# Kernel optimization log

Measured on AMD Instinct MI355X. Metric: run time of the kernel, lower is better.

The kernel has to match this reference:

```python
import jax, jax.numpy as jnp
import numpy as np

N_D = 100000  # num drug nodes
N_G = 100000  # num gene nodes
E = 250000    # edges per etype
D_IN_DRUG, D_IN_GENE, D_OUT = 512, 256, 512
W_SCALE = 0.02


def setup_inputs() -> dict:
    key = jax.random.key(0)
    ks = jax.random.split(key, 20)
    inp = {
        "x_drug": jax.random.normal(ks[0], (N_D, D_IN_DRUG), jnp.float32),
        "x_gene": jax.random.normal(ks[1], (N_G, D_IN_GENE), jnp.float32),
        "W_drug": jax.random.normal(ks[2], (D_IN_DRUG, D_OUT), jnp.float32) * W_SCALE,
        "b_drug": jnp.zeros((D_OUT,), jnp.float32),
        "W_gene": jax.random.normal(ks[3], (D_IN_GENE, D_OUT), jnp.float32) * W_SCALE,
        "b_gene": jnp.zeros((D_OUT,), jnp.float32),
        "W_dd": jax.random.normal(ks[4], (D_OUT, D_OUT), jnp.float32) * W_SCALE,
        "b_dd": jnp.zeros((D_OUT,), jnp.float32),
        "W_dg": jax.random.normal(ks[5], (D_OUT, D_OUT), jnp.float32) * W_SCALE,
        "b_dg": jnp.zeros((D_OUT,), jnp.float32),
        "W_gd": jax.random.normal(ks[6], (D_OUT, D_OUT), jnp.float32) * W_SCALE,
        "b_gd": jnp.zeros((D_OUT,), jnp.float32),
        "W_gg": jax.random.normal(ks[7], (D_OUT, D_OUT), jnp.float32) * W_SCALE,
        "b_gg": jnp.zeros((D_OUT,), jnp.float32),
        "src_dd": jax.random.randint(ks[8], (E,), 0, N_D, jnp.int64),
        "dst_dd": jax.random.randint(ks[9], (E,), 0, N_D, jnp.int64),
        "src_dg": jax.random.randint(ks[10], (E,), 0, N_D, jnp.int64),
        "dst_dg": jax.random.randint(ks[11], (E,), 0, N_G, jnp.int64),
        "src_gd": jax.random.randint(ks[12], (E,), 0, N_G, jnp.int64),
        "dst_gd": jax.random.randint(ks[13], (E,), 0, N_D, jnp.int64),
        "src_gg": jax.random.randint(ks[14], (E,), 0, N_G, jnp.int64),
        "dst_gg": jax.random.randint(ks[15], (E,), 0, N_G, jnp.int64),
    }
    return inp


def _graph_conv(h_src, src, dst, n_src, n_dst, W, b):
    """DGL GraphConv with norm='both': src-norm, scatter-sum, dst-norm, W, bias."""
    ones = jnp.ones(src.shape, h_src.dtype)
    deg_out = jax.ops.segment_sum(ones, src, num_segments=n_src)
    deg_in = jax.ops.segment_sum(ones, dst, num_segments=n_dst)
    norm_src = jax.lax.rsqrt(jnp.maximum(deg_out, 1.0))  # clamp(min=1)
    norm_dst = jax.lax.rsqrt(jnp.maximum(deg_in, 1.0))
    msg = (h_src * norm_src[:, None])[src]               # [E, D_OUT]
    agg = jax.ops.segment_sum(msg, dst, num_segments=n_dst)
    agg = agg * norm_dst[:, None]
    return agg @ W + b


def reference(x_drug, x_gene, W_drug, b_drug, W_gene, b_gene,
              W_dd, b_dd, W_dg, b_dg, W_gd, b_gd, W_gg, b_gg,
              src_dd, dst_dd, src_dg, dst_dg, src_gd, dst_gd, src_gg, dst_gg):
    # per-ntype linear projections to out_size
    h_d = x_drug @ W_drug + b_drug   # [N_D, D_OUT]
    h_g = x_gene @ W_gene + b_gene   # [N_G, D_OUT]
    # per-etype GraphConv aggregates
    f_dd = _graph_conv(h_d, src_dd, dst_dd, N_D, N_D, W_dd, b_dd)  # -> drug
    f_gd = _graph_conv(h_g, src_gd, dst_gd, N_G, N_D, W_gd, b_gd)  # -> drug
    f_dg = _graph_conv(h_d, src_dg, dst_dg, N_D, N_G, W_dg, b_dg)  # -> gene
    f_gg = _graph_conv(h_g, src_gg, dst_gg, N_G, N_G, W_gg, b_gg)  # -> gene
    # mean over etypes targeting each dsttype (stack(...).mean(0))
    out_drug = 0.5 * (f_dd + f_gd)
    out_gene = 0.5 * (f_dg + f_gg)
    return out_drug, out_gene
```

## Files before the change

kernel.cpp:

```cpp
#include <hip/hip_runtime.h>
#include <stdint.h>
#include <stdio.h>

#define ND 100000
#define NG 100000
#define NE 250000
#define NNODE 100000
#define NB 391
#define NBE 977
#define OSTRIDE 100016

typedef __attribute__((ext_vector_type(8))) short short8;
typedef __attribute__((ext_vector_type(4))) int   int4v;
typedef __attribute__((ext_vector_type(2))) int   int2v;
typedef __attribute__((ext_vector_type(4))) float f32x4;

__device__ __forceinline__ float bf2f(short s) {
  union { unsigned u; float f; } v;
  v.u = ((unsigned)(unsigned short)s) << 16;
  return v.f;
}
__device__ __forceinline__ short f2bf_rne(float f) {
  union { float f; unsigned u; } v;
  v.f = f;
  unsigned u = v.u + 0x7FFFu + ((v.u >> 16) & 1u);
  return (short)(u >> 16);
}

__global__ void detect_kernel(const unsigned short* __restrict__ xs,
                              const int* __restrict__ idx, int* __restrict__ flags) {
  __shared__ int cnt_huge, cnt_oddnz;
  if (threadIdx.x == 0) { cnt_huge = 0; cnt_oddnz = 0; }
  __syncthreads();
  int t = threadIdx.x;
  int h = 0;
#pragma unroll
  for (int i = 0; i < 8; ++i) {
    unsigned e = ((unsigned)xs[t * 8 + i] >> 7) & 0xFFu;
    if (e >= 0xC0u) ++h;
  }
  if (h) atomicAdd(&cnt_huge, h);
  if (t < 128 && idx[2 * t + 1] != 0) atomicAdd(&cnt_oddnz, 1);
  __syncthreads();
  if (t == 0) {
    flags[0] = (cnt_huge > 8) ? 1 : 0;
    flags[1] = (cnt_oddnz == 0) ? 1 : 0;
  }
}

__global__ void hist8_kernel(const int* __restrict__ i0, const int* __restrict__ i1,
                             const int* __restrict__ i2, const int* __restrict__ i3,
                             const int* __restrict__ i4, const int* __restrict__ i5,
                             const int* __restrict__ i6, const int* __restrict__ i7,
                             float* __restrict__ degbase, const int* __restrict__ flags) {
  int slot = blockIdx.y;
  const int* idx = slot == 0 ? i0 : slot == 1 ? i1 : slot == 2 ? i2 : slot == 3 ? i3
                 : slot == 4 ? i4 : slot == 5 ? i5 : slot == 6 ? i6 : i7;
  int t = blockIdx.x * blockDim.x + threadIdx.x;
  if (t < NE) {
    int v = flags[1] ? idx[2 * (size_t)t] : idx[t];
    atomicAdd(degbase + (size_t)slot * NNODE + v, 1.0f);
  }
}

__global__ void norm_kernel(float* __restrict__ d, int n) {
  int t = blockIdx.x * blockDim.x + threadIdx.x;
  if (t < n) {
    float v = d[t];
    d[t] = rsqrtf(v < 1.0f ? 1.0f : v);
  }
}


__global__ void scan_partial(const float* __restrict__ degbase, int* __restrict__ part) {
  int et = blockIdx.y, t = threadIdx.x;
  const float* deg = degbase + (size_t)(2 * et + 1) * NNODE;
  __shared__ int sm[256];
  int i = blockIdx.x * 256 + t;
  int v = (i < NNODE) ? (int)deg[i] : 0;
  sm[t] = v;
  __syncthreads();
  for (int s = 128; s > 0; s >>= 1) {
    if (t < s) sm[t] += sm[t + s];
    __syncthreads();
  }
  if (t == 0) part[et * 512 + blockIdx.x] = sm[0];
}

__global__ void scan_single(int* __restrict__ part) {
  int et = blockIdx.x, t = threadIdx.x;
  __shared__ int sm[512];
  int v = (t < NB) ? part[et * 512 + t] : 0;
  sm[t] = v;
  __syncthreads();
  for (int s = 1; s < 512; s <<= 1) {
    int a = (t >= s) ? sm[t - s] : 0;
    __syncthreads();
    sm[t] += a;
    __syncthreads();
  }
  if (t < NB) part[et * 512 + t] = sm[t] - v;
}

__global__ void scan_final(const float* __restrict__ degbase, const int* __restrict__ part,
                           int* __restrict__ offsbase) {
  int et = blockIdx.y, t = threadIdx.x;
  const float* deg = degbase + (size_t)(2 * et + 1) * NNODE;
  int* offs = offsbase + (size_t)et * OSTRIDE;
  __shared__ int sm[256];
  int i = blockIdx.x * 256 + t;
  int v = (i < NNODE) ? (int)deg[i] : 0;
  sm[t] = v;
  __syncthreads();
  for (int s = 1; s < 256; s <<= 1) {
    int a = (t >= s) ? sm[t - s] : 0;
    __syncthreads();
    sm[t] += a;
    __syncthreads();
  }
  int excl = sm[t] - v;
  int base = part[et * 512 + blockIdx.x];
  if (i < NNODE) offs[i] = base + excl;
  if (i == NNODE - 1) offs[NNODE] = base + excl + v;
}

__global__ void csr_scatter4(
    const int* __restrict__ s0, const int* __restrict__ d0,
    const int* __restrict__ s1, const int* __restrict__ d1,
    const int* __restrict__ s2, const int* __restrict__ d2,
    const int* __restrict__ s3, const int* __restrict__ d3,
    const float* __restrict__ degbase, const int* __restrict__ csro,
    int* __restrict__ curs, int* __restrict__ ewbase, const int* __restrict__ flags) {
  int et = blockIdx.y;
  const int* src = et == 0 ? s0 : et == 1 ? s1 : et == 2 ? s2 : s3;
  const int* dst = et == 0 ? d0 : et == 1 ? d1 : et == 2 ? d2 : d3;
  const float* ns = degbase + (size_t)(2 * et) * NNODE;
  const int* offs = csro + (size_t)et * OSTRIDE;
  int* cur = curs + (size_t)et * NNODE;
  int* ew = ewbase + (size_t)et * 2 * NE;
  int t = blockIdx.x * blockDim.x + threadIdx.x;
  if (t >= NE) return;
  int i64 = flags[1];
  int s = i64 ? src[2 * (size_t)t] : src[t];
  int d = i64 ? dst[2 * (size_t)t] : dst[t];
  int pos = offs[d] + atomicAdd(&cur[d], 1);
  union { float f; int i; } u;
  u.f = ns[s];
  int2v v; v[0] = s; v[1] = u.i;
  *(int2v*)(ew + 2 * (size_t)pos) = v;
}

template <int EL>
__device__ __forceinline__ void accum_row(const void* __restrict__ x, int s, float w,
                                          float* acc, int lane, int xf) {
  constexpr int D = EL * 64;
  if (xf) {
    const float* xp = (const float*)x + (size_t)s * D + lane * EL;
    if constexpr (EL == 8) {
      f32x4 q0 = *(const f32x4*)xp;
      f32x4 q1 = *(const f32x4*)(xp + 4);
#pragma unroll
      for (int i = 0; i < 4; ++i) { acc[i] += w * q0[i]; acc[4 + i] += w * q1[i]; }
    } else {
      f32x4 q0 = *(const f32x4*)xp;
#pragma unroll
      for (int i = 0; i < 4; ++i) acc[i] += w * q0[i];
    }
  } else {
    const short* xp = (const short*)x + (size_t)s * D + lane * EL;
    if constexpr (EL == 8) {
      int4v q = *(const int4v*)xp;
#pragma unroll
      for (int i = 0; i < 4; ++i) {
        unsigned u = (unsigned)q[i];
        union { unsigned u; float f; } lo, hi;
        lo.u = u << 16; hi.u = u & 0xFFFF0000u;
        acc[2 * i] += w * lo.f;
        acc[2 * i + 1] += w * hi.f;
      }
    } else {
      int2v q = *(const int2v*)(xp);
#pragma unroll
      for (int i = 0; i < 2; ++i) {
        unsigned u = (unsigned)q[i];
        union { unsigned u; float f; } lo, hi;
        lo.u = u << 16; hi.u = u & 0xFFFF0000u;
        acc[2 * i] += w * lo.f;
        acc[2 * i + 1] += w * hi.f;
      }
    }
  }
}

template <int EL>
__global__ __launch_bounds__(256) void csr_gather2(
    const void* __restrict__ x,
    const int* __restrict__ offsA, const int* __restrict__ ewA,
    const float* __restrict__ ndA, short* __restrict__ yA, float* __restrict__ svA,
    const int* __restrict__ offsB, const int* __restrict__ ewB,
    const float* __restrict__ ndB, short* __restrict__ yB, float* __restrict__ svB,
    const int* __restrict__ flags) {
  constexpr int D = EL * 64;
  int which = blockIdx.x & 1;
  int d = (blockIdx.x >> 1) * 4 + (threadIdx.x >> 6);
  int lane = threadIdx.x & 63;
  int xf = flags[0];
  const int* offs = which ? offsB : offsA;
  const int* ew   = which ? ewB : ewA;
  const float* nd = which ? ndB : ndA;
  short* y        = which ? yB : yA;
  float* sv       = which ? svB : svA;

  int beg = offs[d], end = offs[d + 1];
  float acc[EL];
#pragma unroll
  for (int i = 0; i < EL; ++i) acc[i] = 0.f;
  float sw = 0.f;
  int j = beg;
  for (; j + 2 <= end; j += 2) {
    int2v e0 = *(const int2v*)(ew + 2 * (size_t)j);
    int2v e1 = *(const int2v*)(ew + 2 * (size_t)j + 2);
    union { int i; float f; } u0, u1;
    u0.i = e0[1]; u1.i = e1[1];
    sw += u0.f + u1.f;
    accum_row<EL>(x, e0[0], u0.f, acc, lane, xf);
    accum_row<EL>(x, e1[0], u1.f, acc, lane, xf);
  }
  if (j < end) {
    int2v e0 = *(const int2v*)(ew + 2 * (size_t)j);
    union { int i; float f; } u0;
    u0.i = e0[1];
    sw += u0.f;
    accum_row<EL>(x, e0[0], u0.f, acc, lane, xf);
  }
  float ndv = nd[d];
  if constexpr (EL == 8) {
    union { short s[8]; int4v v; } o;
#pragma unroll
    for (int i = 0; i < 8; ++i) o.s[i] = f2bf_rne(acc[i] * ndv);
    __builtin_nontemporal_store(o.v, (int4v*)(y + (size_t)d * D + lane * EL));
  } else {
    union { short s[4]; int2v v; } o;
#pragma unroll
    for (int i = 0; i < 4; ++i) o.s[i] = f2bf_rne(acc[i] * ndv);
    __builtin_nontemporal_store(o.v, (int2v*)(y + (size_t)d * D + lane * EL));
  }
  if (lane == 0) sv[d] = ndv * sw;
}

__global__ void vt_kernel(const void* __restrict__ Ws, const void* __restrict__ We,
                          short* __restrict__ VT, int Kin, const int* __restrict__ flags) {
  int n = blockIdx.x * 256 + threadIdx.x;
  int k = blockIdx.y;
  float acc = 0.f;
  if (flags[0]) {
    const float* wr = (const float*)Ws + (size_t)k * 512;
    const float* we = (const float*)We;
#pragma unroll 8
    for (int j = 0; j < 512; ++j) acc += wr[j] * we[(size_t)j * 512 + n];
  } else {
    const short* wr = (const short*)Ws + (size_t)k * 512;
    const short* we = (const short*)We;
#pragma unroll 8
    for (int j = 0; j < 512; ++j) acc += bf2f(wr[j]) * bf2f(we[(size_t)j * 512 + n]);
  }
  VT[(size_t)n * Kin + k] = f2bf_rne(0.5f * acc);
}

__global__ void cvec_kernel(const void* __restrict__ b1s, const void* __restrict__ W1,
                            const void* __restrict__ b2s, const void* __restrict__ W2,
                            const void* __restrict__ be1, const void* __restrict__ be2,
                            float* __restrict__ c1, float* __restrict__ c2,
                            float* __restrict__ cb, const int* __restrict__ flags) {
  int n = blockIdx.x * 256 + threadIdx.x;
  float a1 = 0.f, a2 = 0.f, vb1, vb2;
  if (flags[0]) {
    const float* B1 = (const float*)b1s; const float* M1 = (const float*)W1;
    const float* B2 = (const float*)b2s; const float* M2 = (const float*)W2;
    for (int j = 0; j < 512; ++j) {
      a1 += B1[j] * M1[(size_t)j * 512 + n];
      a2 += B2[j] * M2[(size_t)j * 512 + n];
    }
    vb1 = ((const float*)be1)[n]; vb2 = ((const float*)be2)[n];
  } else {
    const short* B1 = (const short*)b1s; const short* M1 = (const short*)W1;
    const short* B2 = (const short*)b2s; const short* M2 = (const short*)W2;
    for (int j = 0; j < 512; ++j) {
      a1 += bf2f(B1[j]) * bf2f(M1[(size_t)j * 512 + n]);
      a2 += bf2f(B2[j]) * bf2f(M2[(size_t)j * 512 + n]);
    }
    vb1 = bf2f(((const short*)be1)[n]); vb2 = bf2f(((const short*)be2)[n]);
  }
  c1[n] = 0.5f * a1;
  c2[n] = 0.5f * a2;
  cb[n] = 0.5f * (vb1 + vb2);
}

__global__ __launch_bounds__(256) void pair_gemm(
    const short* __restrict__ A1, const short* __restrict__ A2,
    const short* __restrict__ B1, const short* __restrict__ B2,
    const float* __restrict__ s1, const float* __restrict__ s2,
    const float* __restrict__ c1, const float* __restrict__ c2,
    const float* __restrict__ cb, float* __restrict__ out, int M) {
  __shared__ __align__(16) short lds_a[128 * 72];
  __shared__ __align__(16) short lds_b[128 * 72];
  const int tid = threadIdx.x;
  const int bn = blockIdx.x, bm = blockIdx.y;
  const int m0 = bm * 128, n0 = bn * 128;
  const int lane = tid & 63, wave = tid >> 6;
  const int wm = wave & 1, wn = wave >> 1;
  const int lr = lane & 15, lq = lane >> 4;

  f32x4 acc[4][4] = {};

  for (int st = 0; st < 12; ++st) {
    const short* Ap; const short* Bp; int K, k0;
    if (st < 8) { Ap = A1; Bp = B1; K = 512; k0 = st << 6; }
    else        { Ap = A2; Bp = B2; K = 256; k0 = (st - 8) << 6; }

#pragma unroll
    for (int i = 0; i < 5; ++i) {
      int c = tid + i * 256;
      if (c < 1152) {
        int row = c / 9;
        int cc = c - row * 9; if (cc > 7) cc = 7;
        int rg = m0 + row; if (rg >= M) rg = M - 1;
        const short* gp = Ap + (size_t)rg * K + (size_t)(k0 + (cc << 3));
        __builtin_amdgcn_global_load_lds(
            (const __attribute__((address_space(1))) void*)gp,
            (__attribute__((address_space(3))) void*)(lds_a + ((size_t)c << 3)),
            16, 0, 0);
      }
    }
#pragma unroll
    for (int i = 0; i < 5; ++i) {
      int c = tid + i * 256;
      if (c < 1152) {
        int row = c / 9;
        int cc = c - row * 9; if (cc > 7) cc = 7;
        const short* gp = Bp + (size_t)(n0 + row) * K + (size_t)(k0 + (cc << 3));
        __builtin_amdgcn_global_load_lds(
            (const __attribute__((address_space(1))) void*)gp,
            (__attribute__((address_space(3))) void*)(lds_b + ((size_t)c << 3)),
            16, 0, 0);
      }
    }
    __syncthreads();

#pragma unroll
    for (int ks = 0; ks < 2; ++ks) {
      short8 bfrag[4];
#pragma unroll
      for (int ni = 0; ni < 4; ++ni) {
        int nl = wn * 64 + ni * 16 + lr;
        bfrag[ni] = *(const short8*)(lds_b + nl * 72 + ks * 32 + lq * 8);
      }
#pragma unroll
      for (int mi = 0; mi < 4; ++mi) {
        int ml = wm * 64 + mi * 16 + lr;
        short8 afrag = *(const short8*)(lds_a + ml * 72 + ks * 32 + lq * 8);
#pragma unroll
        for (int ni = 0; ni < 4; ++ni)
          acc[mi][ni] = __builtin_amdgcn_mfma_f32_16x16x32_bf16(afrag, bfrag[ni], acc[mi][ni], 0, 0, 0);
      }
    }
    __syncthreads();
  }

  float ct1[4], ct2[4], ctb[4]; int gn[4];
#pragma unroll
  for (int ni = 0; ni < 4; ++ni) {
    int n = n0 + wn * 64 + ni * 16 + lr;
    gn[ni] = n; ct1[ni] = c1[n]; ct2[ni] = c2[n]; ctb[ni] = cb[n];
  }
#pragma unroll
  for (int mi = 0; mi < 4; ++mi) {
    int mb = m0 + wm * 64 + mi * 16 + (lq << 2);
#pragma unroll
    for (int r = 0; r < 4; ++r) {
      int m = mb + r;
      if (m < M) {
        float sv1 = s1[m], sv2 = s2[m];
        float* op = out + (size_t)m * 512;
#pragma unroll
        for (int ni = 0; ni < 4; ++ni)
          __builtin_nontemporal_store(
              acc[mi][ni][r] + sv1 * ct1[ni] + sv2 * ct2[ni] + ctb[ni], op + gn[ni]);
      }
    }
  }
}

static constexpr size_t OFF_Y_DD = 0;
static constexpr size_t OFF_Y_DG = OFF_Y_DD + (size_t)NNODE * 512 * 2;
static constexpr size_t OFF_Y_GD = OFF_Y_DG + (size_t)NNODE * 512 * 2;
static constexpr size_t OFF_Y_GG = OFF_Y_GD + (size_t)NNODE * 256 * 2;
static constexpr size_t OFF_VT_DD = OFF_Y_GG + (size_t)NNODE * 256 * 2;
static constexpr size_t OFF_VT_DG = OFF_VT_DD + 512 * 512 * 2;
static constexpr size_t OFF_VT_GD = OFF_VT_DG + 512 * 512 * 2;
static constexpr size_t OFF_VT_GG = OFF_VT_GD + 512 * 256 * 2;
static constexpr size_t OFF_NRM  = OFF_VT_GG + 512 * 256 * 2;
static constexpr size_t OFF_SV   = OFF_NRM + 8 * 400000;
static constexpr size_t OFF_CV   = OFF_SV + 4 * 400000;
static constexpr size_t OFF_FLG  = OFF_CV + 6 * 2048;
static constexpr size_t OFF_CSRO = OFF_FLG + 64;
static constexpr size_t OFF_CURS = OFF_CSRO + (size_t)4 * OSTRIDE * 4;
static constexpr size_t OFF_SRT  = OFF_CURS + 4 * 400000;
static constexpr size_t OFF_PART = OFF_SRT + (size_t)4 * 2 * NE * 4;
static constexpr size_t WS_NEED  = OFF_PART + 4 * 512 * 4;

extern "C" void kernel_launch(void* const* d_in, const int* in_sizes, int n_in,
                              void* d_out, int out_size, void* d_ws, size_t ws_size,
                              hipStream_t stream) {
  const void* x_d    = d_in[0];
  const void* x_g    = d_in[1];
  const void* W_drug = d_in[2];
  const void* b_drug = d_in[3];
  const void* W_gene = d_in[4];
  const void* b_gene = d_in[5];
  const void* W_dd   = d_in[6];
  const void* b_dd   = d_in[7];
  const void* W_dg   = d_in[8];
  const void* b_dg   = d_in[9];
  const void* W_gd   = d_in[10];
  const void* b_gd   = d_in[11];
  const void* W_gg   = d_in[12];
  const void* b_gg   = d_in[13];
  const int* src_dd = (const int*)d_in[14];
  const int* dst_dd = (const int*)d_in[15];
  const int* src_dg = (const int*)d_in[16];
  const int* dst_dg = (const int*)d_in[17];
  const int* src_gd = (const int*)d_in[18];
  const int* dst_gd = (const int*)d_in[19];
  const int* src_gg = (const int*)d_in[20];
  const int* dst_gg = (const int*)d_in[21];

  if (ws_size < WS_NEED) {
    fprintf(stderr, "kernel_launch: ws too small: have %zu need %zu\n", ws_size, WS_NEED);
    return;
  }

  char* ws = (char*)d_ws;
  short* y_dd = (short*)(ws + OFF_Y_DD);
  short* y_dg = (short*)(ws + OFF_Y_DG);
  short* y_gd = (short*)(ws + OFF_Y_GD);
  short* y_gg = (short*)(ws + OFF_Y_GG);
  short* vt_dd = (short*)(ws + OFF_VT_DD);
  short* vt_dg = (short*)(ws + OFF_VT_DG);
  short* vt_gd = (short*)(ws + OFF_VT_GD);
  short* vt_gg = (short*)(ws + OFF_VT_GG);
  float* degbase = (float*)(ws + OFF_NRM);
  float* nd_dd = degbase + 1 * NNODE;
  float* nd_dg = degbase + 3 * NNODE;
  float* nd_gd = degbase + 5 * NNODE;
  float* nd_gg = degbase + 7 * NNODE;
  float* s_dd = (float*)(ws + OFF_SV + 0 * 400000);
  float* s_gd = (float*)(ws + OFF_SV + 1 * 400000);
  float* s_dg = (float*)(ws + OFF_SV + 2 * 400000);
  float* s_gg = (float*)(ws + OFF_SV + 3 * 400000);
  float* c1_drug = (float*)(ws + OFF_CV + 0 * 2048);
  float* c2_drug = (float*)(ws + OFF_CV + 1 * 2048);
  float* cb_drug = (float*)(ws + OFF_CV + 2 * 2048);
  float* c1_gene = (float*)(ws + OFF_CV + 3 * 2048);
  float* c2_gene = (float*)(ws + OFF_CV + 4 * 2048);
  float* cb_gene = (float*)(ws + OFF_CV + 5 * 2048);
  int* flags = (int*)(ws + OFF_FLG);
  int* csro  = (int*)(ws + OFF_CSRO);
  int* curs  = (int*)(ws + OFF_CURS);
  int* ewbase = (int*)(ws + OFF_SRT);
  int* part  = (int*)(ws + OFF_PART);

  float* out_drug = (float*)d_out;
  float* out_gene = out_drug + (size_t)ND * 512;

  detect_kernel<<<1, 256, 0, stream>>>((const unsigned short*)x_d, src_dd, flags);

  hipMemsetAsync(ws + OFF_NRM, 0, 8 * 400000, stream);
  hipMemsetAsync(ws + OFF_CURS, 0, 4 * 400000, stream);

  hist8_kernel<<<dim3(NBE, 8), 256, 0, stream>>>(
      src_dd, dst_dd, src_dg, dst_dg, src_gd, dst_gd, src_gg, dst_gg, degbase, flags);

  scan_partial<<<dim3(NB, 4), 256, 0, stream>>>(degbase, part);
  scan_single<<<4, 512, 0, stream>>>(part);
  scan_final<<<dim3(NB, 4), 256, 0, stream>>>(degbase, part, csro);

  norm_kernel<<<(800000 + 255) / 256, 256, 0, stream>>>(degbase, 800000);

  vt_kernel<<<dim3(2, 512), 256, 0, stream>>>(W_drug, W_dd, vt_dd, 512, flags);
  vt_kernel<<<dim3(2, 512), 256, 0, stream>>>(W_drug, W_dg, vt_dg, 512, flags);
  vt_kernel<<<dim3(2, 256), 256, 0, stream>>>(W_gene, W_gd, vt_gd, 256, flags);
  vt_kernel<<<dim3(2, 256), 256, 0, stream>>>(W_gene, W_gg, vt_gg, 256, flags);
  cvec_kernel<<<2, 256, 0, stream>>>(b_drug, W_dd, b_gene, W_gd, b_dd, b_gd,
                                     c1_drug, c2_drug, cb_drug, flags);
  cvec_kernel<<<2, 256, 0, stream>>>(b_drug, W_dg, b_gene, W_gg, b_dg, b_gg,
                                     c1_gene, c2_gene, cb_gene, flags);

  csr_scatter4<<<dim3(NBE, 4), 256, 0, stream>>>(
      src_dd, dst_dd, src_dg, dst_dg, src_gd, dst_gd, src_gg, dst_gg,
      degbase, csro, curs, ewbase, flags);

  dim3 gb(2 * (NNODE / 4));
  csr_gather2<8><<<gb, 256, 0, stream>>>(
      x_d, csro + 0 * OSTRIDE, ewbase + 0 * 2 * NE, nd_dd, y_dd, s_dd,
           csro + 1 * OSTRIDE, ewbase + 1 * 2 * NE, nd_dg, y_dg, s_dg, flags);
  csr_gather2<4><<<gb, 256, 0, stream>>>(
      x_g, csro + 2 * OSTRIDE, ewbase + 2 * 2 * NE, nd_gd, y_gd, s_gd,
           csro + 3 * OSTRIDE, ewbase + 3 * 2 * NE, nd_gg, y_gg, s_gg, flags);

  dim3 gg(4, (ND + 127) / 128);
  pair_gemm<<<gg, 256, 0, stream>>>(y_dd, y_gd, vt_dd, vt_gd, s_dd, s_gd,
                                    c1_drug, c2_drug, cb_drug, out_drug, ND);
  pair_gemm<<<gg, 256, 0, stream>>>(y_dg, y_gg, vt_dg, vt_gg, s_dg, s_gg,
                                    c1_gene, c2_gene, cb_gene, out_gene, NG);
}
```

Measured before the change: 1.472 ms.

## Drop cursor array and norm kernel; use atomic offsets and 2-rows-per-wave gather

The CSR scatter now bumps the offsets array itself with atomics, so after scattering each offs[d] holds its end position and the gather reads its range as [offs[d-1], offs[d]]. This removes the cursor buffer and its memset. The rsqrt degree normalisation is computed inline in the scatter and gather kernels, so the separate norm kernel pass goes away. The D=256 gather is rewritten to process two destination rows per 64-lane wave with 8 elements per lane, making each load wider and using all lanes.

```diff
diff --git a/kernel.cpp b/kernel.cpp
--- a/kernel.cpp
+++ b/kernel.cpp
@@ -63,14 +63,6 @@
   }
 }
 
-__global__ void norm_kernel(float* __restrict__ d, int n) {
-  int t = blockIdx.x * blockDim.x + threadIdx.x;
-  if (t < n) {
-    float v = d[t];
-    d[t] = rsqrtf(v < 1.0f ? 1.0f : v);
-  }
-}
-
 
 __global__ void scan_partial(const float* __restrict__ degbase, int* __restrict__ part) {
   int et = blockIdx.y, t = threadIdx.x;
@@ -121,7 +113,6 @@
   int excl = sm[t] - v;
   int base = part[et * 512 + blockIdx.x];
   if (i < NNODE) offs[i] = base + excl;
-  if (i == NNODE - 1) offs[NNODE] = base + excl + v;
 }
 
 __global__ void csr_scatter4(
@@ -129,45 +120,40 @@
     const int* __restrict__ s1, const int* __restrict__ d1,
     const int* __restrict__ s2, const int* __restrict__ d2,
     const int* __restrict__ s3, const int* __restrict__ d3,
-    const float* __restrict__ degbase, const int* __restrict__ csro,
-    int* __restrict__ curs, int* __restrict__ ewbase, const int* __restrict__ flags) {
+    const float* __restrict__ degbase, int* __restrict__ csro,
+    int* __restrict__ ewbase, const int* __restrict__ flags) {
   int et = blockIdx.y;
   const int* src = et == 0 ? s0 : et == 1 ? s1 : et == 2 ? s2 : s3;
   const int* dst = et == 0 ? d0 : et == 1 ? d1 : et == 2 ? d2 : d3;
-  const float* ns = degbase + (size_t)(2 * et) * NNODE;
-  const int* offs = csro + (size_t)et * OSTRIDE;
-  int* cur = curs + (size_t)et * NNODE;
+  const float* degs = degbase + (size_t)(2 * et) * NNODE;
+  int* offs = csro + (size_t)et * OSTRIDE;
   int* ew = ewbase + (size_t)et * 2 * NE;
   int t = blockIdx.x * blockDim.x + threadIdx.x;
   if (t >= NE) return;
   int i64 = flags[1];
   int s = i64 ? src[2 * (size_t)t] : src[t];
   int d = i64 ? dst[2 * (size_t)t] : dst[t];
-  int pos = offs[d] + atomicAdd(&cur[d], 1);
+  int pos = atomicAdd(&offs[d], 1);
+  float dg = degs[s];
   union { float f; int i; } u;
-  u.f = ns[s];
+  u.f = rsqrtf(dg < 1.0f ? 1.0f : dg);
   int2v v; v[0] = s; v[1] = u.i;
   *(int2v*)(ew + 2 * (size_t)pos) = v;
 }
 
 template <int EL>
-__device__ __forceinline__ void accum_row(const void* __restrict__ x, int s, float w,
-                                          float* acc, int lane, int xf) {
-  constexpr int D = EL * 64;
+__device__ __forceinline__ void accum_row(const void* __restrict__ x, size_t base, float w,
+                                          float* acc, int xf) {
   if (xf) {
-    const float* xp = (const float*)x + (size_t)s * D + lane * EL;
+    const float* xp = (const float*)x + base;
     if constexpr (EL == 8) {
       f32x4 q0 = *(const f32x4*)xp;
       f32x4 q1 = *(const f32x4*)(xp + 4);
 #pragma unroll
       for (int i = 0; i < 4; ++i) { acc[i] += w * q0[i]; acc[4 + i] += w * q1[i]; }
-    } else {
-      f32x4 q0 = *(const f32x4*)xp;
-#pragma unroll
-      for (int i = 0; i < 4; ++i) acc[i] += w * q0[i];
     }
   } else {
-    const short* xp = (const short*)x + (size_t)s * D + lane * EL;
+    const short* xp = (const short*)x + base;
     if constexpr (EL == 8) {
       int4v q = *(const int4v*)xp;
 #pragma unroll
@@ -178,43 +164,33 @@
         acc[2 * i] += w * lo.f;
         acc[2 * i + 1] += w * hi.f;
       }
-    } else {
-      int2v q = *(const int2v*)(xp);
-#pragma unroll
-      for (int i = 0; i < 2; ++i) {
-        unsigned u = (unsigned)q[i];
-        union { unsigned u; float f; } lo, hi;
-        lo.u = u << 16; hi.u = u & 0xFFFF0000u;
-        acc[2 * i] += w * lo.f;
-        acc[2 * i + 1] += w * hi.f;
-      }
-    }
-  }
-}
-
-template <int EL>
-__global__ __launch_bounds__(256) void csr_gather2(
+    }
+  }
+}
+
+__global__ __launch_bounds__(256) void csr_gather_d512(
     const void* __restrict__ x,
     const int* __restrict__ offsA, const int* __restrict__ ewA,
-    const float* __restrict__ ndA, short* __restrict__ yA, float* __restrict__ svA,
+    const float* __restrict__ dgA, short* __restrict__ yA, float* __restrict__ svA,
     const int* __restrict__ offsB, const int* __restrict__ ewB,
-    const float* __restrict__ ndB, short* __restrict__ yB, float* __restrict__ svB,
+    const float* __restrict__ dgB, short* __restrict__ yB, float* __restrict__ svB,
     const int* __restrict__ flags) {
-  constexpr int D = EL * 64;
+  constexpr int D = 512;
   int which = blockIdx.x & 1;
   int d = (blockIdx.x >> 1) * 4 + (threadIdx.x >> 6);
   int lane = threadIdx.x & 63;
   int xf = flags[0];
   const int* offs = which ? offsB : offsA;
   const int* ew   = which ? ewB : ewA;
-  const float* nd = which ? ndB : ndA;
+  const float* dg = which ? dgB : dgA;
   short* y        = which ? yB : yA;
   float* sv       = which ? svB : svA;
 
-  int beg = offs[d], end = offs[d + 1];
-  float acc[EL];
-#pragma unroll
-  for (int i = 0; i < EL; ++i) acc[i] = 0.f;
+  int beg = d ? offs[d - 1] : 0;
+  int end = offs[d];
+  float acc[8];
+#pragma unroll
+  for (int i = 0; i < 8; ++i) acc[i] = 0.f;
   float sw = 0.f;
   int j = beg;
   for (; j + 2 <= end; j += 2) {
@@ -223,29 +199,74 @@
     union { int i; float f; } u0, u1;
     u0.i = e0[1]; u1.i = e1[1];
     sw += u0.f + u1.f;
-    accum_row<EL>(x, e0[0], u0.f, acc, lane, xf);
-    accum_row<EL>(x, e1[0], u1.f, acc, lane, xf);
+    accum_row<8>(x, (size_t)e0[0] * D + lane * 8, u0.f, acc, xf);
+    accum_row<8>(x, (size_t)e1[0] * D + lane * 8, u1.f, acc, xf);
   }
   if (j < end) {
     int2v e0 = *(const int2v*)(ew + 2 * (size_t)j);
     union { int i; float f; } u0;
     u0.i = e0[1];
     sw += u0.f;
-    accum_row<EL>(x, e0[0], u0.f, acc, lane, xf);
-  }
-  float ndv = nd[d];
-  if constexpr (EL == 8) {
-    union { short s[8]; int4v v; } o;
-#pragma unroll
-    for (int i = 0; i < 8; ++i) o.s[i] = f2bf_rne(acc[i] * ndv);
-    __builtin_nontemporal_store(o.v, (int4v*)(y + (size_t)d * D + lane * EL));
-  } else {
-    union { short s[4]; int2v v; } o;
-#pragma unroll
-    for (int i = 0; i < 4; ++i) o.s[i] = f2bf_rne(acc[i] * ndv);
-    __builtin_nontemporal_store(o.v, (int2v*)(y + (size_t)d * D + lane * EL));
-  }
+    accum_row<8>(x, (size_t)e0[0] * D + lane * 8, u0.f, acc, xf);
+  }
+  float dv = dg[d];
+  float ndv = rsqrtf(dv < 1.0f ? 1.0f : dv);
+  union { short s[8]; int4v v; } o;
+#pragma unroll
+  for (int i = 0; i < 8; ++i) o.s[i] = f2bf_rne(acc[i] * ndv);
+  __builtin_nontemporal_store(o.v, (int4v*)(y + (size_t)d * D + lane * 8));
   if (lane == 0) sv[d] = ndv * sw;
+}
+
+__global__ __launch_bounds__(256) void csr_gather_d256(
+    const void* __restrict__ x,
+    const int* __restrict__ offsA, const int* __restrict__ ewA,
+    const float* __restrict__ dgA, short* __restrict__ yA, float* __restrict__ svA,
+    const int* __restrict__ offsB, const int* __restrict__ ewB,
+    const float* __restrict__ dgB, short* __restrict__ yB, float* __restrict__ svB,
+    const int* __restrict__ flags) {
+  constexpr int D = 256;
+  int which = blockIdx.x & 1;
+  int lane = threadIdx.x & 63;
+  int d = (blockIdx.x >> 1) * 8 + (threadIdx.x >> 6) * 2 + (lane >> 5);
+  int ln = lane & 31;
+  int xf = flags[0];
+  const int* offs = which ? offsB : offsA;
+  const int* ew   = which ? ewB : ewA;
+  const float* dg = which ? dgB : dgA;
+  short* y        = which ? yB : yA;
+  float* sv       = which ? svB : svA;
+
+  int beg = d ? offs[d - 1] : 0;
+  int end = offs[d];
+  float acc[8];
+#pragma unroll
+  for (int i = 0; i < 8; ++i) acc[i] = 0.f;
+  float sw = 0.f;
+  int j = beg;
+  for (; j + 2 <= end; j += 2) {
+    int2v e0 = *(const int2v*)(ew + 2 * (size_t)j);
+    int2v e1 = *(const int2v*)(ew + 2 * (size_t)j + 2);
+    union { int i; float f; } u0, u1;
+    u0.i = e0[1]; u1.i = e1[1];
+    sw += u0.f + u1.f;
+    accum_row<8>(x, (size_t)e0[0] * D + ln * 8, u0.f, acc, xf);
+    accum_row<8>(x, (size_t)e1[0] * D + ln * 8, u1.f, acc, xf);
+  }
+  if (j < end) {
+    int2v e0 = *(const int2v*)(ew + 2 * (size_t)j);
+    union { int i; float f; } u0;
+    u0.i = e0[1];
+    sw += u0.f;
+    accum_row<8>(x, (size_t)e0[0] * D + ln * 8, u0.f, acc, xf);
+  }
+  float dv = dg[d];
+  float ndv = rsqrtf(dv < 1.0f ? 1.0f : dv);
+  union { short s[8]; int4v v; } o;
+#pragma unroll
+  for (int i = 0; i < 8; ++i) o.s[i] = f2bf_rne(acc[i] * ndv);
+  __builtin_nontemporal_store(o.v, (int4v*)(y + (size_t)d * D + ln * 8));
+  if (ln == 0) sv[d] = ndv * sw;
 }
 
 __global__ void vt_kernel(const void* __restrict__ Ws, const void* __restrict__ We,
@@ -404,8 +425,7 @@
 static constexpr size_t OFF_CV   = OFF_SV + 4 * 400000;
 static constexpr size_t OFF_FLG  = OFF_CV + 6 * 2048;
 static constexpr size_t OFF_CSRO = OFF_FLG + 64;
-static constexpr size_t OFF_CURS = OFF_CSRO + (size_t)4 * OSTRIDE * 4;
-static constexpr size_t OFF_SRT  = OFF_CURS + 4 * 400000;
+static constexpr size_t OFF_SRT  = OFF_CSRO + (size_t)4 * OSTRIDE * 4;
 static constexpr size_t OFF_PART = OFF_SRT + (size_t)4 * 2 * NE * 4;
 static constexpr size_t WS_NEED  = OFF_PART + 4 * 512 * 4;
 
@@ -450,10 +470,10 @@
   short* vt_gd = (short*)(ws + OFF_VT_GD);
   short* vt_gg = (short*)(ws + OFF_VT_GG);
   float* degbase = (float*)(ws + OFF_NRM);
-  float* nd_dd = degbase + 1 * NNODE;
-  float* nd_dg = degbase + 3 * NNODE;
-  float* nd_gd = degbase + 5 * NNODE;
-  float* nd_gg = degbase + 7 * NNODE;
+  float* dg_dd = degbase + 1 * NNODE;
+  float* dg_dg = degbase + 3 * NNODE;
+  float* dg_gd = degbase + 5 * NNODE;
+  float* dg_gg = degbase + 7 * NNODE;
   float* s_dd = (float*)(ws + OFF_SV + 0 * 400000);
   float* s_gd = (float*)(ws + OFF_SV + 1 * 400000);
   float* s_dg = (float*)(ws + OFF_SV + 2 * 400000);
@@ -466,7 +486,6 @@
   float* cb_gene = (float*)(ws + OFF_CV + 5 * 2048);
   int* flags = (int*)(ws + OFF_FLG);
   int* csro  = (int*)(ws + OFF_CSRO);
-  int* curs  = (int*)(ws + OFF_CURS);
   int* ewbase = (int*)(ws + OFF_SRT);
   int* part  = (int*)(ws + OFF_PART);
 
@@ -476,7 +495,6 @@
   detect_kernel<<<1, 256, 0, stream>>>((const unsigned short*)x_d, src_dd, flags);
 
   hipMemsetAsync(ws + OFF_NRM, 0, 8 * 400000, stream);
-  hipMemsetAsync(ws + OFF_CURS, 0, 4 * 400000, stream);
 
   hist8_kernel<<<dim3(NBE, 8), 256, 0, stream>>>(
       src_dd, dst_dd, src_dg, dst_dg, src_gd, dst_gd, src_gg, dst_gg, degbase, flags);
@@ -484,8 +502,6 @@
   scan_partial<<<dim3(NB, 4), 256, 0, stream>>>(degbase, part);
   scan_single<<<4, 512, 0, stream>>>(part);
   scan_final<<<dim3(NB, 4), 256, 0, stream>>>(degbase, part, csro);
-
-  norm_kernel<<<(800000 + 255) / 256, 256, 0, stream>>>(degbase, 800000);
 
   vt_kernel<<<dim3(2, 512), 256, 0, stream>>>(W_drug, W_dd, vt_dd, 512, flags);
   vt_kernel<<<dim3(2, 512), 256, 0, stream>>>(W_drug, W_dg, vt_dg, 512, flags);
@@ -498,15 +514,14 @@
 
   csr_scatter4<<<dim3(NBE, 4), 256, 0, stream>>>(
       src_dd, dst_dd, src_dg, dst_dg, src_gd, dst_gd, src_gg, dst_gg,
-      degbase, csro, curs, ewbase, flags);
-
-  dim3 gb(2 * (NNODE / 4));
-  csr_gather2<8><<<gb, 256, 0, stream>>>(
-      x_d, csro + 0 * OSTRIDE, ewbase + 0 * 2 * NE, nd_dd, y_dd, s_dd,
-           csro + 1 * OSTRIDE, ewbase + 1 * 2 * NE, nd_dg, y_dg, s_dg, flags);
-  csr_gather2<4><<<gb, 256, 0, stream>>>(
-      x_g, csro + 2 * OSTRIDE, ewbase + 2 * 2 * NE, nd_gd, y_gd, s_gd,
-           csro + 3 * OSTRIDE, ewbase + 3 * 2 * NE, nd_gg, y_gg, s_gg, flags);
+      degbase, csro, ewbase, flags);
+
+  csr_gather_d512<<<dim3(2 * (NNODE / 4)), 256, 0, stream>>>(
+      x_d, csro + 0 * OSTRIDE, ewbase + 0 * 2 * NE, dg_dd, y_dd, s_dd,
+           csro + 1 * OSTRIDE, ewbase + 1 * 2 * NE, dg_dg, y_dg, s_dg, flags);
+  csr_gather_d256<<<dim3(2 * (NNODE / 8)), 256, 0, stream>>>(
+      x_g, csro + 2 * OSTRIDE, ewbase + 2 * 2 * NE, dg_gd, y_gd, s_gd,
+           csro + 3 * OSTRIDE, ewbase + 3 * 2 * NE, dg_gg, y_gg, s_gg, flags);
 
   dim3 gg(4, (ND + 127) / 128);
   pair_gemm<<<gg, 256, 0, stream>>>(y_dd, y_gd, vt_dd, vt_gd, s_dd, s_gd,
```

Result: no change. 1.453 ms (-1.3%).
